# Kernel optimization log

Measured on AMD Instinct MI355X. Metric: run time of the kernel, lower is better.

Reference implementation:

```python
import jax, jax.numpy as jnp
import numpy as np

GRID_H, GRID_W = 24, 24
N_BASE_ACTIONS = 6
B = 131072


def setup_inputs() -> dict:
    key = jax.random.key(0)
    k1, k2, k3 = jax.random.split(key, 3)
    logits = jax.random.normal(k1, (GRID_H, GRID_W), dtype=jnp.float32)
    monoaction_mask = jax.random.randint(k2, (B, GRID_H, GRID_W), 0, 2).astype(jnp.bool_)
    monofield_base_converter = jax.random.randint(k3, (GRID_H, GRID_W), 0, N_BASE_ACTIONS, dtype=jnp.int32)
    return {
        "logits": logits,
        "monoaction_mask": monoaction_mask,
        "monofield_base_converter": monofield_base_converter,
    }


def reference(logits, monoaction_mask, monofield_base_converter):
    # scale: divide sap action (last) by 225
    scale = jnp.ones((1, N_BASE_ACTIONS), dtype=jnp.float32).at[:, -1].set(225.0)
    # one-hot grouping of grid cells into base actions: (H, W, N)
    onehot = (monofield_base_converter[..., None]
              == jnp.arange(N_BASE_ACTIONS, dtype=jnp.int32)).astype(logits.dtype)
    m = monoaction_mask.astype(logits.dtype)  # (B, H, W)
    # grouped masked sum over grid, equivalent to sum(where=mask) in original
    masked_logits = jnp.einsum('bhw,hwn->bn', m * logits[None, :, :], onehot)  # (B, N)
    counts = jnp.einsum('bhw,hwn->bn', m, onehot)  # (B, N)
    any_mask = counts > 0  # == jnp.any(mask, axis=(-3,-2)) in original
    masked_logits = masked_logits / scale
    masked_logits = jnp.where(any_mask, masked_logits, jnp.finfo(jnp.float32).min)
    # if no valid cell at all for this unit, force logit[0] = 1.0
    any_unit = jnp.any(monoaction_mask, axis=(-2, -1))  # (B,)
    masked_logits = jnp.where(any_unit[..., None], masked_logits,
                              masked_logits.at[..., 0].set(1.0))
    return masked_logits
```

## Files before the change

### kernel.cpp

```cpp
#include <hip/hip_runtime.h>


typedef short bf16x8 __attribute__((ext_vector_type(8)));
typedef float f32x4 __attribute__((ext_vector_type(4)));
typedef unsigned uint4n __attribute__((ext_vector_type(4)));

union U4S8 { uint4n u; bf16x8 s; };

__device__ inline unsigned short f2bf(float f) {
  unsigned u = __builtin_bit_cast(unsigned, f);
  u += 0x7FFFu + ((u >> 16) & 1u);
  return (unsigned short)(u >> 16);
}

__device__ inline unsigned short wval(const float* __restrict__ logits,
                                      const int* __restrict__ conv,
                                      int cell, int n) {
  if (n > 12) return 0;
  if (n == 12) return 0x3F80;
  int g = conv[cell];
  if (n < 6) return (g == n) ? f2bf(logits[cell]) : (unsigned short)0;
  return (g == n - 6) ? (unsigned short)0x3F80 : (unsigned short)0;
}

__device__ inline void cvt_pair(unsigned x, unsigned& lo, unsigned& hi) {
  lo = (x & 0x00010001u) * 0x3F80u;
  hi = ((x >> 8) & 0x00010001u) * 0x3F80u;
}

__global__ __launch_bounds__(256) void head_kernel(
    const float* __restrict__ logits,
    const unsigned char* __restrict__ mask,
    const int* __restrict__ conv,
    float* __restrict__ out,
    int ntiles) {
  __shared__ __align__(16) unsigned short wt[18 * 64 * 8];
  __shared__ int votes[4];

  int tid = threadIdx.x;
  const unsigned* mask_dw = (const unsigned*)mask;

  unsigned long long bad = __ballot(mask_dw[tid] > 1u);
  if ((tid & 63) == 0) votes[tid >> 6] = (bad != 0ull);
  __syncthreads();
  int flag = !(votes[0] | votes[1] | votes[2] | votes[3]);

  if (flag) {
#pragma unroll 2
    for (int i = 0; i < 36; ++i) {
      int e = tid + i * 256;
      int j = e & 7, l = (e >> 3) & 63, kt = e >> 9;
      int cell = kt * 32 + (l >> 4) * 8 + j;
      wt[e] = wval(logits, conv, cell, l & 15);
    }
  } else {
#pragma unroll 2
    for (int i = 0; i < 36; ++i) {
      int e = tid + i * 256;
      int j = e & 7, l = (e >> 3) & 63, f = e >> 9;
      int pj = (j & 4) | ((j & 1) << 1) | ((j & 2) >> 1);
      int cell = (f >> 1) * 64 + (l >> 4) * 16 + (f & 1) * 8 + pj;
      wt[e] = wval(logits, conv, cell, l & 15);
    }
  }
  __syncthreads();

  int lane = tid & 63;
  int tile = blockIdx.x * 4 + (tid >> 6);
  if (tile >= ntiles) return;

  int m = lane & 15;
  int q = lane >> 4;
  size_t tb = (size_t)tile * 16;
  const bf16x8* wl = (const bf16x8*)wt;

  f32x4 acc = {0.f, 0.f, 0.f, 0.f};

  if (flag) {
    const unsigned* mp = mask_dw + (tb + (size_t)m) * 576 + q * 8;
#pragma unroll 3
    for (int kt = 0; kt < 18; ++kt) {
      uint4n u = __builtin_nontemporal_load((const uint4n*)(mp + kt * 32));
      uint4n w = __builtin_nontemporal_load((const uint4n*)(mp + kt * 32 + 4));
      U4S8 a;
      a.u = (uint4n){(u.x | (u.y << 16)) * 0x3F80u,
                     (u.z | (u.w << 16)) * 0x3F80u,
                     (w.x | (w.y << 16)) * 0x3F80u,
                     (w.z | (w.w << 16)) * 0x3F80u};
      acc = __builtin_amdgcn_mfma_f32_16x16x32_bf16(a.s, wl[kt * 64 + lane],
                                                    acc, 0, 0, 0);
    }
  } else {
    const unsigned char* ap = mask + (tb + (size_t)m) * 576 + q * 16;
#pragma unroll 3
    for (int kt = 0; kt < 9; ++kt) {
      uint4n av = __builtin_nontemporal_load((const uint4n*)(ap + kt * 64));
      U4S8 a0, a1;
      unsigned l0, h0, l1, h1;
      cvt_pair(av.x, l0, h0); cvt_pair(av.y, l1, h1);
      a0.u = (uint4n){l0, h0, l1, h1};
      cvt_pair(av.z, l0, h0); cvt_pair(av.w, l1, h1);
      a1.u = (uint4n){l0, h0, l1, h1};
      acc = __builtin_amdgcn_mfma_f32_16x16x32_bf16(a0.s, wl[(2 * kt) * 64 + lane],
                                                    acc, 0, 0, 0);
      acc = __builtin_amdgcn_mfma_f32_16x16x32_bf16(a1.s, wl[(2 * kt + 1) * 64 + lane],
                                                    acc, 0, 0, 0);
    }
  }

  int col = m;
  int srcCnt = (lane & 48) + ((col < 6) ? (col + 6) : 0);
  int srcTot = (lane & 48) + 12;
  float scale = (col == 5) ? (1.0f / 225.0f) : 1.0f;
  const float FMIN = -3.4028234663852886e38f;

#pragma unroll
  for (int r = 0; r < 4; ++r) {
    float s   = acc[r];
    float cnt = __shfl(s, srcCnt);
    float tot = __shfl(s, srcTot);
    if (col < 6) {
      float o;
      if (tot < 0.5f)       o = (col == 0) ? 1.0f : FMIN;
      else if (cnt > 0.5f)  o = s * scale;
      else                  o = FMIN;
      size_t b = tb + (size_t)q * 4 + r;
      out[b * 6 + col] = o;
    }
  }
}

extern "C" void kernel_launch(void* const* d_in, const int* in_sizes, int n_in,
                              void* d_out, int out_size, void* d_ws, size_t ws_size,
                              hipStream_t stream) {
  const float*          logits = (const float*)d_in[0];
  const unsigned char*  mask   = (const unsigned char*)d_in[1];
  const int*            conv   = (const int*)d_in[2];
  float*                out    = (float*)d_out;

  int B = in_sizes[1] / 576;
  int ntiles = B / 16;
  int blocks = (ntiles + 3) / 4;

  head_kernel<<<blocks, 256, 0, stream>>>(logits, mask, conv, out, ntiles);
}
```

Baseline: 403.8 us.

## Process two row tiles per wave and batch mask loads up front

Each wave now handles two 16-row tiles instead of one, which halves the grid and amortizes the per-block LDS weight-table setup over twice the work. In the byte-mask path, all nine 16-byte loads for both tiles are issued before any MFMA so more memory requests are in flight, and the B fragments from LDS are shared between the two accumulators. Launch bounds now request 4 blocks per CU. The cost is higher register pressure from holding 18 vector loads, and fewer blocks for latency hiding.

```diff
diff --git a/kernel.cpp b/kernel.cpp
--- a/kernel.cpp
+++ b/kernel.cpp
@@ -28,7 +28,7 @@
   hi = ((x >> 8) & 0x00010001u) * 0x3F80u;
 }
 
-__global__ __launch_bounds__(256) void head_kernel(
+__global__ __launch_bounds__(256, 4) void head_kernel(
     const float* __restrict__ logits,
     const unsigned char* __restrict__ mask,
     const int* __restrict__ conv,
@@ -66,45 +66,79 @@
   __syncthreads();
 
   int lane = tid & 63;
-  int tile = blockIdx.x * 4 + (tid >> 6);
-  if (tile >= ntiles) return;
+  int t0 = (blockIdx.x * 4 + (tid >> 6)) * 2;
+  if (t0 >= ntiles) return;
+  bool two = (t0 + 1) < ntiles;
 
   int m = lane & 15;
   int q = lane >> 4;
-  size_t tb = (size_t)tile * 16;
+  size_t tb0 = (size_t)t0 * 16;
   const bf16x8* wl = (const bf16x8*)wt;
 
-  f32x4 acc = {0.f, 0.f, 0.f, 0.f};
+  f32x4 acc0 = {0.f, 0.f, 0.f, 0.f};
+  f32x4 acc1 = {0.f, 0.f, 0.f, 0.f};
 
   if (flag) {
-    const unsigned* mp = mask_dw + (tb + (size_t)m) * 576 + q * 8;
+    const unsigned* mp0 = mask_dw + (tb0 + (size_t)m) * 576 + q * 8;
 #pragma unroll 3
     for (int kt = 0; kt < 18; ++kt) {
-      uint4n u = __builtin_nontemporal_load((const uint4n*)(mp + kt * 32));
-      uint4n w = __builtin_nontemporal_load((const uint4n*)(mp + kt * 32 + 4));
+      uint4n u = __builtin_nontemporal_load((const uint4n*)(mp0 + kt * 32));
+      uint4n w = __builtin_nontemporal_load((const uint4n*)(mp0 + kt * 32 + 4));
       U4S8 a;
       a.u = (uint4n){(u.x | (u.y << 16)) * 0x3F80u,
                      (u.z | (u.w << 16)) * 0x3F80u,
                      (w.x | (w.y << 16)) * 0x3F80u,
                      (w.z | (w.w << 16)) * 0x3F80u};
-      acc = __builtin_amdgcn_mfma_f32_16x16x32_bf16(a.s, wl[kt * 64 + lane],
-                                                    acc, 0, 0, 0);
+      acc0 = __builtin_amdgcn_mfma_f32_16x16x32_bf16(a.s, wl[kt * 64 + lane],
+                                                     acc0, 0, 0, 0);
+    }
+    if (two) {
+      const unsigned* mp1 = mp0 + 16 * 576;
+#pragma unroll 3
+      for (int kt = 0; kt < 18; ++kt) {
+        uint4n u = __builtin_nontemporal_load((const uint4n*)(mp1 + kt * 32));
+        uint4n w = __builtin_nontemporal_load((const uint4n*)(mp1 + kt * 32 + 4));
+        U4S8 a;
+        a.u = (uint4n){(u.x | (u.y << 16)) * 0x3F80u,
+                       (u.z | (u.w << 16)) * 0x3F80u,
+                       (w.x | (w.y << 16)) * 0x3F80u,
+                       (w.z | (w.w << 16)) * 0x3F80u};
+        acc1 = __builtin_amdgcn_mfma_f32_16x16x32_bf16(a.s, wl[kt * 64 + lane],
+                                                       acc1, 0, 0, 0);
+      }
     }
   } else {
-    const unsigned char* ap = mask + (tb + (size_t)m) * 576 + q * 16;
-#pragma unroll 3
+    const unsigned char* ap0 = mask + (tb0 + (size_t)m) * 576 + q * 16;
+    const unsigned char* ap1 = ap0 + 16 * 576;
+    uint4n av0[9], av1[9];
+#pragma unroll
+    for (int kt = 0; kt < 9; ++kt)
+      av0[kt] = __builtin_nontemporal_load((const uint4n*)(ap0 + kt * 64));
+    if (two) {
+#pragma unroll
+      for (int kt = 0; kt < 9; ++kt)
+        av1[kt] = __builtin_nontemporal_load((const uint4n*)(ap1 + kt * 64));
+    }
+#pragma unroll
     for (int kt = 0; kt < 9; ++kt) {
-      uint4n av = __builtin_nontemporal_load((const uint4n*)(ap + kt * 64));
+      bf16x8 b0 = wl[(2 * kt) * 64 + lane];
+      bf16x8 b1 = wl[(2 * kt + 1) * 64 + lane];
       U4S8 a0, a1;
       unsigned l0, h0, l1, h1;
-      cvt_pair(av.x, l0, h0); cvt_pair(av.y, l1, h1);
+      cvt_pair(av0[kt].x, l0, h0); cvt_pair(av0[kt].y, l1, h1);
       a0.u = (uint4n){l0, h0, l1, h1};
-      cvt_pair(av.z, l0, h0); cvt_pair(av.w, l1, h1);
+      cvt_pair(av0[kt].z, l0, h0); cvt_pair(av0[kt].w, l1, h1);
       a1.u = (uint4n){l0, h0, l1, h1};
-      acc = __builtin_amdgcn_mfma_f32_16x16x32_bf16(a0.s, wl[(2 * kt) * 64 + lane],
-                                                    acc, 0, 0, 0);
-      acc = __builtin_amdgcn_mfma_f32_16x16x32_bf16(a1.s, wl[(2 * kt + 1) * 64 + lane],
-                                                    acc, 0, 0, 0);
+      acc0 = __builtin_amdgcn_mfma_f32_16x16x32_bf16(a0.s, b0, acc0, 0, 0, 0);
+      acc0 = __builtin_amdgcn_mfma_f32_16x16x32_bf16(a1.s, b1, acc0, 0, 0, 0);
+      if (two) {
+        cvt_pair(av1[kt].x, l0, h0); cvt_pair(av1[kt].y, l1, h1);
+        a0.u = (uint4n){l0, h0, l1, h1};
+        cvt_pair(av1[kt].z, l0, h0); cvt_pair(av1[kt].w, l1, h1);
+        a1.u = (uint4n){l0, h0, l1, h1};
+        acc1 = __builtin_amdgcn_mfma_f32_16x16x32_bf16(a0.s, b0, acc1, 0, 0, 0);
+        acc1 = __builtin_amdgcn_mfma_f32_16x16x32_bf16(a1.s, b1, acc1, 0, 0, 0);
+      }
     }
   }
 
@@ -116,7 +150,7 @@
 
 #pragma unroll
   for (int r = 0; r < 4; ++r) {
-    float s   = acc[r];
+    float s   = acc0[r];
     float cnt = __shfl(s, srcCnt);
     float tot = __shfl(s, srcTot);
     if (col < 6) {
@@ -124,8 +158,24 @@
       if (tot < 0.5f)       o = (col == 0) ? 1.0f : FMIN;
       else if (cnt > 0.5f)  o = s * scale;
       else                  o = FMIN;
-      size_t b = tb + (size_t)q * 4 + r;
+      size_t b = tb0 + (size_t)q * 4 + r;
       out[b * 6 + col] = o;
+    }
+  }
+  if (two) {
+#pragma unroll
+    for (int r = 0; r < 4; ++r) {
+      float s   = acc1[r];
+      float cnt = __shfl(s, srcCnt);
+      float tot = __shfl(s, srcTot);
+      if (col < 6) {
+        float o;
+        if (tot < 0.5f)       o = (col == 0) ? 1.0f : FMIN;
+        else if (cnt > 0.5f)  o = s * scale;
+        else                  o = FMIN;
+        size_t b = tb0 + 16 + (size_t)q * 4 + r;
+        out[b * 6 + col] = o;
+      }
     }
   }
 }
@@ -140,7 +190,8 @@
 
   int B = in_sizes[1] / 576;
   int ntiles = B / 16;
-  int blocks = (ntiles + 3) / 4;
+  int npair = (ntiles + 1) / 2;
+  int blocks = (npair + 3) / 4;
 
   head_kernel<<<blocks, 256, 0, stream>>>(logits, mask, conv, out, ntiles);
 }
```

New measurement: 394.6 us. 2.3% less time.

## Process four tiles per wave and batch mask loads to amortize weight setup

Applied to the files above, without the earlier changes.

Each wave now handles four 16-row tiles instead of one, so the grid shrinks fourfold. The per-block LDS weight table build and flag vote are spread over more work. In the byte-mask path all 36 loads per lane are issued up front, and each B fragment read from LDS is reused across four MFMAs, giving more memory parallelism. The cost is much higher register pressure (launch bounds of 2 blocks per CU) and fewer blocks to hide latency.

```diff
diff --git a/kernel.cpp b/kernel.cpp
--- a/kernel.cpp
+++ b/kernel.cpp
@@ -28,7 +28,7 @@
   hi = ((x >> 8) & 0x00010001u) * 0x3F80u;
 }
 
-__global__ __launch_bounds__(256) void head_kernel(
+__global__ __launch_bounds__(256, 2) void head_kernel(
     const float* __restrict__ logits,
     const unsigned char* __restrict__ mask,
     const int* __restrict__ conv,
@@ -66,45 +66,63 @@
   __syncthreads();
 
   int lane = tid & 63;
-  int tile = blockIdx.x * 4 + (tid >> 6);
-  if (tile >= ntiles) return;
+  int t0 = (blockIdx.x * 4 + (tid >> 6)) * 4;
+  if (t0 >= ntiles) return;
 
   int m = lane & 15;
   int q = lane >> 4;
-  size_t tb = (size_t)tile * 16;
+  size_t tb0 = (size_t)t0 * 16;
   const bf16x8* wl = (const bf16x8*)wt;
 
-  f32x4 acc = {0.f, 0.f, 0.f, 0.f};
+  f32x4 acc[4];
+#pragma unroll
+  for (int t = 0; t < 4; ++t) acc[t] = (f32x4){0.f, 0.f, 0.f, 0.f};
 
   if (flag) {
-    const unsigned* mp = mask_dw + (tb + (size_t)m) * 576 + q * 8;
+#pragma unroll
+    for (int t = 0; t < 4; ++t) {
+      if (t0 + t >= ntiles) continue;
+      const unsigned* mp = mask_dw + (tb0 + (size_t)t * 16 + (size_t)m) * 576 + q * 8;
 #pragma unroll 3
-    for (int kt = 0; kt < 18; ++kt) {
-      uint4n u = __builtin_nontemporal_load((const uint4n*)(mp + kt * 32));
-      uint4n w = __builtin_nontemporal_load((const uint4n*)(mp + kt * 32 + 4));
-      U4S8 a;
-      a.u = (uint4n){(u.x | (u.y << 16)) * 0x3F80u,
-                     (u.z | (u.w << 16)) * 0x3F80u,
-                     (w.x | (w.y << 16)) * 0x3F80u,
-                     (w.z | (w.w << 16)) * 0x3F80u};
-      acc = __builtin_amdgcn_mfma_f32_16x16x32_bf16(a.s, wl[kt * 64 + lane],
-                                                    acc, 0, 0, 0);
+      for (int kt = 0; kt < 18; ++kt) {
+        uint4n u = __builtin_nontemporal_load((const uint4n*)(mp + kt * 32));
+        uint4n w = __builtin_nontemporal_load((const uint4n*)(mp + kt * 32 + 4));
+        U4S8 a;
+        a.u = (uint4n){(u.x | (u.y << 16)) * 0x3F80u,
+                       (u.z | (u.w << 16)) * 0x3F80u,
+                       (w.x | (w.y << 16)) * 0x3F80u,
+                       (w.z | (w.w << 16)) * 0x3F80u};
+        acc[t] = __builtin_amdgcn_mfma_f32_16x16x32_bf16(a.s, wl[kt * 64 + lane],
+                                                         acc[t], 0, 0, 0);
+      }
     }
   } else {
-    const unsigned char* ap = mask + (tb + (size_t)m) * 576 + q * 16;
-#pragma unroll 3
+    const unsigned char* ap = mask + (tb0 + (size_t)m) * 576 + q * 16;
+    uint4n av[4][9];
+#pragma unroll
+    for (int t = 0; t < 4; ++t) {
+      if (t0 + t >= ntiles) continue;
+#pragma unroll
+      for (int kt = 0; kt < 9; ++kt)
+        av[t][kt] = __builtin_nontemporal_load(
+            (const uint4n*)(ap + t * 9216 + kt * 64));
+    }
+#pragma unroll
     for (int kt = 0; kt < 9; ++kt) {
-      uint4n av = __builtin_nontemporal_load((const uint4n*)(ap + kt * 64));
-      U4S8 a0, a1;
-      unsigned l0, h0, l1, h1;
-      cvt_pair(av.x, l0, h0); cvt_pair(av.y, l1, h1);
-      a0.u = (uint4n){l0, h0, l1, h1};
-      cvt_pair(av.z, l0, h0); cvt_pair(av.w, l1, h1);
-      a1.u = (uint4n){l0, h0, l1, h1};
-      acc = __builtin_amdgcn_mfma_f32_16x16x32_bf16(a0.s, wl[(2 * kt) * 64 + lane],
-                                                    acc, 0, 0, 0);
-      acc = __builtin_amdgcn_mfma_f32_16x16x32_bf16(a1.s, wl[(2 * kt + 1) * 64 + lane],
-                                                    acc, 0, 0, 0);
+      bf16x8 b0 = wl[(2 * kt) * 64 + lane];
+      bf16x8 b1 = wl[(2 * kt + 1) * 64 + lane];
+#pragma unroll
+      for (int t = 0; t < 4; ++t) {
+        if (t0 + t >= ntiles) continue;
+        U4S8 a0, a1;
+        unsigned l0, h0, l1, h1;
+        cvt_pair(av[t][kt].x, l0, h0); cvt_pair(av[t][kt].y, l1, h1);
+        a0.u = (uint4n){l0, h0, l1, h1};
+        cvt_pair(av[t][kt].z, l0, h0); cvt_pair(av[t][kt].w, l1, h1);
+        a1.u = (uint4n){l0, h0, l1, h1};
+        acc[t] = __builtin_amdgcn_mfma_f32_16x16x32_bf16(a0.s, b0, acc[t], 0, 0, 0);
+        acc[t] = __builtin_amdgcn_mfma_f32_16x16x32_bf16(a1.s, b1, acc[t], 0, 0, 0);
+      }
     }
   }
 
@@ -115,17 +133,21 @@
   const float FMIN = -3.4028234663852886e38f;
 
 #pragma unroll
-  for (int r = 0; r < 4; ++r) {
-    float s   = acc[r];
-    float cnt = __shfl(s, srcCnt);
-    float tot = __shfl(s, srcTot);
-    if (col < 6) {
-      float o;
-      if (tot < 0.5f)       o = (col == 0) ? 1.0f : FMIN;
-      else if (cnt > 0.5f)  o = s * scale;
-      else                  o = FMIN;
-      size_t b = tb + (size_t)q * 4 + r;
-      out[b * 6 + col] = o;
+  for (int t = 0; t < 4; ++t) {
+    if (t0 + t >= ntiles) continue;
+#pragma unroll
+    for (int r = 0; r < 4; ++r) {
+      float s   = acc[t][r];
+      float cnt = __shfl(s, srcCnt);
+      float tot = __shfl(s, srcTot);
+      if (col < 6) {
+        float o;
+        if (tot < 0.5f)       o = (col == 0) ? 1.0f : FMIN;
+        else if (cnt > 0.5f)  o = s * scale;
+        else                  o = FMIN;
+        size_t b = tb0 + (size_t)t * 16 + (size_t)q * 4 + r;
+        out[b * 6 + col] = o;
+      }
     }
   }
 }
@@ -140,7 +162,7 @@
 
   int B = in_sizes[1] / 576;
   int ntiles = B / 16;
-  int blocks = (ntiles + 3) / 4;
+  int blocks = (ntiles + 15) / 16;
 
   head_kernel<<<blocks, 256, 0, stream>>>(logits, mask, conv, out, ntiles);
 }
```

Result: faster. 393.4 us (median of 2 runs) (-2.6%).
